# Kernel tuning notes

Hardware: AMD Instinct MI355X
Metric: run time of the kernel (lower is better)

## Reference

```python
import jax, jax.numpy as jnp
import numpy as np


def _seg_softmax(z, seg, num_seg):
    # PyG-style softmax over segments (numerically stable)
    m = jax.ops.segment_max(z, seg, num_segments=num_seg)
    e = jnp.exp(z - m[seg])
    s = jax.ops.segment_sum(e, seg, num_segments=num_seg)
    return e / s[seg]


def _structure(x, W, b, edge_index, batch):
    """Eager (numpy) watershed structure: peaks + level-synchronous BFS fill.
    Faithful to Clusterer.forward/fill: peaks are nodes whose elevation >= all
    in-neighbors; BFS expands along descending edges, a node joins the
    cluster(s) of whichever frontier origins reach it first (ties -> all),
    and is never re-assigned afterwards. Index structure is non-differentiable
    (matches torch autograd semantics)."""
    x = np.asarray(x); W = np.asarray(W); b = np.asarray(b)
    ei = np.asarray(edge_index); batch = np.asarray(batch)
    N = x.shape[0]; B = int(batch.max()) + 1
    # elevation = softmax(Linear(x), batch)
    z = (x @ W.T).ravel() + b[0]
    m = np.full(B, -np.inf, dtype=np.float64); np.maximum.at(m, batch, z)
    e = np.exp(z - m[batch]); s = np.zeros(B); np.add.at(s, batch, e)
    elev = e / s[batch]
    src, dst = ei[0], ei[1]
    # peaks: every incoming edge (src->dst) has elev[dst] >= elev[src]
    deg = np.bincount(dst, minlength=N)
    ge = np.bincount(dst[elev[dst] >= elev[src]], minlength=N)
    peaks = np.nonzero(ge == deg)[0]  # sorted, includes isolated nodes
    # descending edges only
    dmask = elev[dst] <= elev[src]
    ds, dd = src[dmask], dst[dmask]
    mems_list = [peaks]; ids_list = [peaks]
    visited = np.zeros(N, dtype=bool); visited[peaks] = True
    fn, fc = peaks, peaks  # frontier (node, cluster-id) pairs
    while fn.size:
        order = np.argsort(fn, kind='stable')
        fcs = fc[order]
        counts = np.bincount(fn, minlength=N)
        starts = np.concatenate([np.zeros(1, np.int64), np.cumsum(counts)])
        emask = counts[ds] > 0
        es, ed = ds[emask], dd[emask]
        rep = counts[es]
        tot = int(rep.sum())
        if tot == 0:
            break
        # attribute each descent edge to every cluster id of its origin
        base = np.repeat(starts[es], rep)
        grp = np.cumsum(rep) - rep
        within = np.arange(tot) - np.repeat(grp, rep)
        nc = fcs[base + within]
        nd = np.repeat(ed, rep)
        keep = ~visited[nd]  # nodes already in a cluster are never re-assigned
        nd, nc = nd[keep], nc[keep]
        if nd.size == 0:
            break
        pairs = np.unique(np.stack([nd, nc], axis=1), axis=0)
        nd, nc = pairs[:, 0], pairs[:, 1]
        visited[nd] = True
        mems_list.append(nd); ids_list.append(nc)
        fn, fc = nd, nc
    mems = np.concatenate(mems_list)
    ids = np.concatenate(ids_list)
    new_ids = np.searchsorted(peaks, ids)  # relabel peak node ids -> 0..P-1
    cluster_batch = batch[peaks]
    return mems, new_ids, peaks, cluster_batch, int(peaks.size), B


def setup_inputs() -> dict:
    rng = np.random.default_rng(0)
    N, C, B = 100000, 256, 8
    Ng = N // B
    Eu = 800000  # undirected edge draws, ~avg degree 16 after symmetrization
    g = rng.integers(0, B, Eu)
    s = g * Ng + rng.integers(0, Ng, Eu)
    d = g * Ng + rng.integers(0, Ng, Eu)
    keep = s != d
    s, d = s[keep], d[keep]
    src = np.concatenate([s, d]); dst = np.concatenate([d, s])
    key = src * N + dst
    _, idx = np.unique(key, return_index=True)  # coalesce (sorted, deduped)
    edge_index = np.stack([src[idx], dst[idx]]).astype(np.int64)
    batch = np.repeat(np.arange(B), Ng).astype(np.int64)
    x = rng.standard_normal((N, C)).astype(np.float32)
    W = (rng.standard_normal((1, C)) * 0.05).astype(np.float32)
    b = np.zeros((1,), np.float32)
    return {"x": jnp.asarray(x), "edge_index": jnp.asarray(edge_index),
            "batch": jnp.asarray(batch), "W": jnp.asarray(W), "b": jnp.asarray(b)}


def reference(x, edge_index, batch, W, b):
    mems, ids, peaks, cbatch, P, B = _structure(x, W, b, edge_index, batch)
    mems_j = jnp.asarray(mems); ids_j = jnp.asarray(ids); cb = jnp.asarray(cbatch)
    # differentiable pooling math (TopoPool.get_elevations + TopoPool.scale)
    z = (x @ W.T)[:, 0] + b[0]                       # [N]
    elev = _seg_softmax(z, batch, B)                  # per-graph softmax
    max_elev = jax.ops.segment_max(elev[mems_j], ids_j, num_segments=P)   # [P]
    max_x = jax.ops.segment_max(x[mems_j], ids_j, num_segments=P)        # [P,C]
    normed = _seg_softmax(max_elev, cb, B)            # softmax over clusters per graph
    pooled = max_x * normed[:, None]                  # [P,C]
    return pooled, cb, elev
```

## Files before the change

### kernel.cpp

```cpp
#include <hip/hip_runtime.h>
#include <hip/hip_bf16.h>
#include <stdint.h>


#define LINF 0x3FFFFFFF
#define MAXL 60
#define LSPLIT 10
#define NGMAX 12544
#define TAILCAP 8192

__device__ __forceinline__ unsigned encf(float f) {
  unsigned u = __float_as_uint(f);
  return (u & 0x80000000u) ? ~u : (u | 0x80000000u);
}
__device__ __forceinline__ float decf(unsigned u) {
  unsigned v = (u & 0x80000000u) ? (u & 0x7fffffffu) : ~u;
  return __uint_as_float(v);
}
__device__ __forceinline__ float bf2f(unsigned h) {
  return __uint_as_float(h << 16);
}
__device__ __forceinline__ unsigned f2bf(float f) {
  unsigned u = __float_as_uint(f);
  return (u + 0x7FFFu + ((u >> 16) & 1u)) >> 16;
}

__global__ void k_z(const float* __restrict__ x, const float* __restrict__ W,
                    const float* __restrict__ b, const int* __restrict__ batch,
                    float* __restrict__ z, unsigned* __restrict__ bmax_enc,
                    unsigned short* __restrict__ M, int N, int C) {
  __shared__ unsigned smax[8];
  if (threadIdx.x < 8) smax[threadIdx.x] = 0u;
  __syncthreads();
  int lane = threadIdx.x & 63;
  int wid = threadIdx.x >> 6;
  int chunk = (N + gridDim.x - 1) / gridDim.x;
  int v0 = blockIdx.x * chunk;
  int v1 = min(v0 + chunk, N);
  float b0 = b[0];
  for (int v = v0 + (wid << 2); v < v1; v += 16) {
    int nv = min(4, v1 - v);
    float acc[4] = {0.f, 0.f, 0.f, 0.f};
    for (int f = lane * 4; f < C; f += 256) {
      float4 xv[4];
      #pragma unroll
      for (int k = 0; k < 4; ++k) {
        int vv = v + (k < nv ? k : 0);
        xv[k] = *(const float4*)(x + (size_t)vv * C + f);
      }
      float4 wv = *(const float4*)(W + f);
      #pragma unroll
      for (int k = 0; k < 4; ++k) {
        acc[k] += xv[k].x * wv.x + xv[k].y * wv.y + xv[k].z * wv.z + xv[k].w * wv.w;
      }
      #pragma unroll
      for (int k = 0; k < 4; ++k) {
        if (k < nv) {
          uint2 pk;
          pk.x = f2bf(xv[k].x) | (f2bf(xv[k].y) << 16);
          pk.y = f2bf(xv[k].z) | (f2bf(xv[k].w) << 16);
          *(uint2*)(M + (size_t)(v + k) * C + f) = pk;
        }
      }
    }
    #pragma unroll
    for (int off = 32; off > 0; off >>= 1) {
      acc[0] += __shfl_xor(acc[0], off, 64);
      acc[1] += __shfl_xor(acc[1], off, 64);
      acc[2] += __shfl_xor(acc[2], off, 64);
      acc[3] += __shfl_xor(acc[3], off, 64);
    }
    if (lane < nv) {
      float zv = acc[lane] + b0;
      z[v + lane] = zv;
      atomicMax(&smax[batch[v + lane] & 7], encf(zv));
    }
  }
  __syncthreads();
  if (threadIdx.x < 8)
    if (smax[threadIdx.x]) atomicMax(&bmax_enc[threadIdx.x], smax[threadIdx.x]);
}

__global__ void k_e(const float* __restrict__ z, const int* __restrict__ batch,
                    const unsigned* __restrict__ bmax_enc, float* __restrict__ e,
                    float* __restrict__ bsum, int N) {
  __shared__ float ssum[1024];
  for (int i = threadIdx.x; i < 1024; i += blockDim.x) ssum[i] = 0.f;
  __syncthreads();
  int i = blockIdx.x * blockDim.x + threadIdx.x;
  if (i < N) {
    int bt = batch[i] & 1023;
    float ev = expf(z[i] - decf(bmax_enc[bt]));
    e[i] = ev;
    atomicAdd(&ssum[bt], ev);
  }
  __syncthreads();
  for (int t = threadIdx.x; t < 1024; t += blockDim.x)
    if (ssum[t] != 0.f) atomicAdd(&bsum[t], ssum[t]);
}

__global__ void k_edges(const int* __restrict__ ei, const float* __restrict__ z,
                        int* __restrict__ notpeak, int* __restrict__ desc_cnt,
                        const float* __restrict__ e, const float* __restrict__ bsum,
                        const int* __restrict__ batch, float* __restrict__ elev_out,
                        int E, int N) {
  int i = blockIdx.x * blockDim.x + threadIdx.x;
  if (i < N) elev_out[i] = e[i] / bsum[batch[i] & 1023];
  if (i >= E) return;
  int s = ei[i], d = ei[E + i];
  float zs = z[s], zd = z[d];
  if (zd < zs) notpeak[d] = 1;
  if (zd <= zs) atomicAdd(&desc_cnt[s], 1);
}

__global__ void k_chunksum2(const int* __restrict__ desc_cnt, const int* __restrict__ notpeak,
                            int n, int* __restrict__ csA, int* __restrict__ csB) {
  __shared__ int sA[512], sB[512];
  int t = threadIdx.x;
  int i = blockIdx.x * 512 + t;
  int a = 0, bb = 0;
  if (i < n) { a = desc_cnt[i]; bb = (notpeak[i] == 0) ? 1 : 0; }
  sA[t] = a; sB[t] = bb;
  __syncthreads();
  for (int off = 256; off > 0; off >>= 1) {
    if (t < off) { sA[t] += sA[t + off]; sB[t] += sB[t + off]; }
    __syncthreads();
  }
  if (t == 0) { csA[blockIdx.x] = sA[0]; csB[blockIdx.x] = sB[0]; }
}

__global__ void k_chunkscan2(int* __restrict__ csA, int* __restrict__ csB, int nchunks) {
  __shared__ int sA[1024], sB[1024];
  int t = threadIdx.x;
  int vA = (t < nchunks) ? csA[t] : 0;
  int vB = (t < nchunks) ? csB[t] : 0;
  sA[t] = vA; sB[t] = vB;
  __syncthreads();
  for (int off = 1; off < 1024; off <<= 1) {
    int aA = (t >= off) ? sA[t - off] : 0;
    int aB = (t >= off) ? sB[t - off] : 0;
    __syncthreads();
    sA[t] += aA; sB[t] += aB;
    __syncthreads();
  }
  if (t < nchunks) { csA[t] = sA[t] - vA; csB[t] = sB[t] - vB; }
}

__global__ void k_offsets(const int* __restrict__ vals, const int* __restrict__ chunkoff,
                          int2* __restrict__ ocp, int* __restrict__ cursor, int n) {
  __shared__ int s[512];
  int t = threadIdx.x;
  int i = blockIdx.x * 512 + t;
  int v = (i < n) ? vals[i] : 0;
  s[t] = v;
  __syncthreads();
  for (int off = 1; off < 512; off <<= 1) {
    int add = (t >= off) ? s[t - off] : 0;
    __syncthreads();
    s[t] += add;
    __syncthreads();
  }
  if (i < n) {
    int excl = s[t] - v + chunkoff[blockIdx.x];
    ocp[i] = make_int2(excl, excl);
    cursor[i] = excl;
  }
}

__global__ void k_peak_emit(const int* __restrict__ notpeak, const int* __restrict__ chunkoff,
                            const int* __restrict__ batch, const float* __restrict__ elev,
                            int* __restrict__ peaklist, int* __restrict__ cbatch,
                            float* __restrict__ out_cb, float* __restrict__ melev,
                            int n, int P) {
  __shared__ int s[512];
  int t = threadIdx.x;
  int i = blockIdx.x * 512 + t;
  int v = (i < n) ? (notpeak[i] == 0 ? 1 : 0) : 0;
  s[t] = v;
  __syncthreads();
  for (int off = 1; off < 512; off <<= 1) {
    int add = (t >= off) ? s[t - off] : 0;
    __syncthreads();
    s[t] += add;
    __syncthreads();
  }
  if (i < n && v) {
    int r = s[t] - 1 + chunkoff[blockIdx.x];
    if (r < P) {
      peaklist[r] = i;
      int bt = batch[i];
      cbatch[r] = bt;
      out_cb[r] = (float)bt;
      melev[r] = elev[i];
    }
  }
}

__global__ void k_fill(const int* __restrict__ ei, const float* __restrict__ z,
                       int* __restrict__ cursor, int* __restrict__ adj, int E) {
  int i = blockIdx.x * blockDim.x + threadIdx.x;
  if (i >= E) return;
  int s = ei[i], d = ei[E + i];
  if (z[d] <= z[s]) {
    int pos = atomicAdd(&cursor[s], 1);
    adj[pos] = d;
  }
}

__global__ void __launch_bounds__(1024, 1)
k_levels(const int* __restrict__ adj, const int2* __restrict__ ocp,
         const int* __restrict__ desc_cnt, const int* __restrict__ notpeak,
         int* __restrict__ level, int* __restrict__ lnodes,
         int* __restrict__ qend_g, int Ng, int N) {
  __shared__ int lvl[NGMAX];
  __shared__ unsigned short lq[NGMAX];
  __shared__ int soff[NGMAX + 1];
  __shared__ int s_qcnt[64];
  __shared__ int qend_s[64];
  const int b = blockIdx.x, base = b * Ng;
  const int tid = threadIdx.x, nth = blockDim.x;

  if (tid < 64) s_qcnt[tid] = 0;
  __syncthreads();
  for (int i = tid; i < Ng; i += nth) {
    soff[i] = ocp[base + i].x;
    bool pk = (notpeak[base + i] == 0);
    lvl[i] = pk ? 0 : LINF;
    if (pk) { int p = atomicAdd(&s_qcnt[0], 1); lq[p] = (unsigned short)i; }
  }
  if (tid == 0)
    soff[Ng] = (base + Ng < N) ? ocp[base + Ng].x : (ocp[N - 1].x + desc_cnt[N - 1]);
  __syncthreads();
  int qb = 0, qe = s_qcnt[0];
  int L = 0;
  while (L < MAXL && qe > qb) {
    if (tid == 0) qend_s[L] = qe;
    int units = (qe - qb) << 2;
    for (int t = tid; t < units; t += nth) {
      int qi = qb + (t >> 2), sub = t & 3;
      int lu = (int)lq[qi];
      int o = soff[lu], oe = soff[lu + 1];
      int j = o + sub;
      if (j < oe) {
        int w0 = adj[j];
        for (;;) {
          int jn = j + 4;
          int w1 = (jn < oe) ? adj[jn] : 0;
          int wl = w0 - base;
          if (lvl[wl] == LINF) {
            int old = atomicMin(&lvl[wl], L + 1);
            if (old == LINF) {
              int p = qe + atomicAdd(&s_qcnt[L + 1], 1);
              lq[p] = (unsigned short)wl;
            }
          }
          if (jn >= oe) break;
          w0 = w1; j = jn;
        }
      }
    }
    __syncthreads();
    int produced = s_qcnt[L + 1];
    qb = qe; qe += produced; ++L;
  }
  if (tid == 0) {
    for (int l = L; l < 63; ++l) qend_s[l] = qe;
    qend_s[63] = L;
  }
  __syncthreads();
  if (tid < 64) qend_g[b * 64 + tid] = qend_s[tid];
  for (int i = tid; i < Ng; i += nth) level[base + i] = lvl[i];
  for (int qi = tid; qi < qe; qi += nth) lnodes[base + qi] = (int)lq[qi];
}

__global__ void k_filter(const int* __restrict__ ei, const float* __restrict__ z,
                         const int* __restrict__ level, int2* __restrict__ ocp,
                         int* __restrict__ adj, int E) {
  int i = blockIdx.x * blockDim.x + threadIdx.x;
  if (i >= E) return;
  int s = ei[i], d = ei[E + i];
  if (z[d] <= z[s] && level[d] == level[s] + 1) {
    int pos = atomicAdd(&ocp[s].y, 1);
    adj[pos] = d;
  }
}

__global__ void __launch_bounds__(1024, 1)
k_dp_deep(const int* __restrict__ lnodes, const int* __restrict__ qend_g,
          const int2* __restrict__ ocp, const int* __restrict__ adj,
          unsigned short* __restrict__ M, int Ng, int C) {
  __shared__ unsigned short lqd[TAILCAP];
  __shared__ int2 soc[TAILCAP];
  __shared__ int qend_s[64];
  const int b = blockIdx.x, base = b * Ng;
  const int tid = threadIdx.x, nth = blockDim.x;
  if (tid < 64) qend_s[tid] = qend_g[b * 64 + tid];
  __syncthreads();
  const int Lmax = qend_s[63];
  if (Lmax - 1 < LSPLIT) return;
  const int ts = qend_s[LSPLIT - 1];
  const int qe = qend_s[62];
  const int tn = qe - ts;
  const bool useCache = (tn > 0) && (tn <= TAILCAP);
  if (useCache) {
    for (int i = tid; i < tn; i += nth) {
      int lid = lnodes[base + ts + i];
      lqd[i] = (unsigned short)lid;
      soc[i] = ocp[base + lid];
    }
  }
  __syncthreads();
  const int lane = tid & 31, hw = tid >> 5, nhw = nth >> 5;
  for (int L2 = Lmax - 1; L2 >= LSPLIT; --L2) {
    int sL = qend_s[L2 - 1], eL = qend_s[L2];
    for (int p = sL + hw; p < eL; p += nhw) {
      int u, o, e2;
      if (useCache) { u = base + (int)lqd[p - ts]; int2 v = soc[p - ts]; o = v.x; e2 = v.y; }
      else          { int lid = lnodes[base + p]; u = base + lid; int2 v = ocp[u]; o = v.x; e2 = v.y; }
      if (e2 == o) continue;
      uint4 sq = ((const uint4*)(M + (size_t)u * C))[lane];
      float4 a0, a1;
      a0.x = bf2f(sq.x & 0xffffu); a0.y = bf2f(sq.x >> 16);
      a0.z = bf2f(sq.y & 0xffffu); a0.w = bf2f(sq.y >> 16);
      a1.x = bf2f(sq.z & 0xffffu); a1.y = bf2f(sq.z >> 16);
      a1.z = bf2f(sq.w & 0xffffu); a1.w = bf2f(sq.w >> 16);
      for (int j = o; j < e2; ++j) {
        int wn = adj[j];
        uint4 q = ((const uint4*)(M + (size_t)wn * C))[lane];
        a0.x = fmaxf(a0.x, bf2f(q.x & 0xffffu));
        a0.y = fmaxf(a0.y, bf2f(q.x >> 16));
        a0.z = fmaxf(a0.z, bf2f(q.y & 0xffffu));
        a0.w = fmaxf(a0.w, bf2f(q.y >> 16));
        a1.x = fmaxf(a1.x, bf2f(q.z & 0xffffu));
        a1.y = fmaxf(a1.y, bf2f(q.z >> 16));
        a1.z = fmaxf(a1.z, bf2f(q.w & 0xffffu));
        a1.w = fmaxf(a1.w, bf2f(q.w >> 16));
      }
      uint4 pk4;
      pk4.x = f2bf(a0.x) | (f2bf(a0.y) << 16);
      pk4.y = f2bf(a0.z) | (f2bf(a0.w) << 16);
      pk4.z = f2bf(a1.x) | (f2bf(a1.y) << 16);
      pk4.w = f2bf(a1.z) | (f2bf(a1.w) << 16);
      ((uint4*)(M + (size_t)u * C))[lane] = pk4;
    }
    __syncthreads();
  }
}

__global__ void __launch_bounds__(256)
k_dp(const int* __restrict__ lnodes, const int* __restrict__ qend,
     const int* __restrict__ adj, const int2* __restrict__ ocp,
     unsigned short* __restrict__ M, int L, int C, int Ng) {
  const int b = blockIdx.y;
  int lane = threadIdx.x & 31;
  int ghw = (blockIdx.x * blockDim.x + threadIdx.x) >> 5;
  int nhw = (gridDim.x * blockDim.x) >> 5;
  int s = L ? qend[b * 64 + L - 1] : 0;
  int e = qend[b * 64 + L];
  for (int idx = s + ghw; idx < e; idx += nhw) {
    int u = b * Ng + lnodes[b * Ng + idx];
    int2 oc2 = ocp[u];
    int o = oc2.x, oc = oc2.y - oc2.x;
    if (oc == 0) continue;
    uint4 sq = ((const uint4*)(M + (size_t)u * C))[lane];
    float4 a0, a1;
    a0.x = bf2f(sq.x & 0xffffu); a0.y = bf2f(sq.x >> 16);
    a0.z = bf2f(sq.y & 0xffffu); a0.w = bf2f(sq.y >> 16);
    a1.x = bf2f(sq.z & 0xffffu); a1.y = bf2f(sq.z >> 16);
    a1.z = bf2f(sq.w & 0xffffu); a1.w = bf2f(sq.w >> 16);
    for (int j = 0; j < oc; j += 4) {
      int m = oc - j;
      int wn[4];
      #pragma unroll
      for (int k = 0; k < 4; k++) wn[k] = adj[o + j + (k < m ? k : 0)];
      #pragma unroll
      for (int k = 0; k < 4; k++) {
        uint4 q = ((const uint4*)(M + (size_t)wn[k] * C))[lane];
        a0.x = fmaxf(a0.x, bf2f(q.x & 0xffffu));
        a0.y = fmaxf(a0.y, bf2f(q.x >> 16));
        a0.z = fmaxf(a0.z, bf2f(q.y & 0xffffu));
        a0.w = fmaxf(a0.w, bf2f(q.y >> 16));
        a1.x = fmaxf(a1.x, bf2f(q.z & 0xffffu));
        a1.y = fmaxf(a1.y, bf2f(q.z >> 16));
        a1.z = fmaxf(a1.z, bf2f(q.w & 0xffffu));
        a1.w = fmaxf(a1.w, bf2f(q.w >> 16));
      }
    }
    uint4 p;
    p.x = f2bf(a0.x) | (f2bf(a0.y) << 16);
    p.y = f2bf(a0.z) | (f2bf(a0.w) << 16);
    p.z = f2bf(a1.x) | (f2bf(a1.y) << 16);
    p.w = f2bf(a1.z) | (f2bf(a1.w) << 16);
    ((uint4*)(M + (size_t)u * C))[lane] = p;
  }
}

__global__ void k_cnorm(const float* __restrict__ melev, const int* __restrict__ cbatch,
                        float* __restrict__ normed, int P) {
  __shared__ unsigned cm[1024];
  __shared__ float cs[1024];
  int t = threadIdx.x;
  for (int i = t; i < 1024; i += blockDim.x) { cm[i] = 0u; cs[i] = 0.f; }
  __syncthreads();
  for (int i = t; i < P; i += blockDim.x) atomicMax(&cm[cbatch[i] & 1023], encf(melev[i]));
  __syncthreads();
  for (int i = t; i < P; i += blockDim.x) {
    int bt = cbatch[i] & 1023;
    atomicAdd(&cs[bt], expf(melev[i] - decf(cm[bt])));
  }
  __syncthreads();
  for (int i = t; i < P; i += blockDim.x) {
    int bt = cbatch[i] & 1023;
    normed[i] = expf(melev[i] - decf(cm[bt])) / cs[bt];
  }
}

__global__ void __launch_bounds__(256)
k_dp0_pool(const int* __restrict__ peaklist, const float* __restrict__ normed,
           const int* __restrict__ adj, const int2* __restrict__ ocp,
           const unsigned short* __restrict__ M, float* __restrict__ out,
           int P, int C) {
  int lane = threadIdx.x & 31;
  int ghw = (blockIdx.x * blockDim.x + threadIdx.x) >> 5;
  int nhw = (gridDim.x * blockDim.x) >> 5;
  for (int r = ghw; r < P; r += nhw) {
    int u = peaklist[r];
    int2 oc2 = ocp[u];
    int o = oc2.x, oc = oc2.y - oc2.x;
    uint4 sq = ((const uint4*)(M + (size_t)u * C))[lane];
    float4 a0, a1;
    a0.x = bf2f(sq.x & 0xffffu); a0.y = bf2f(sq.x >> 16);
    a0.z = bf2f(sq.y & 0xffffu); a0.w = bf2f(sq.y >> 16);
    a1.x = bf2f(sq.z & 0xffffu); a1.y = bf2f(sq.z >> 16);
    a1.z = bf2f(sq.w & 0xffffu); a1.w = bf2f(sq.w >> 16);
    for (int j = 0; j < oc; j += 4) {
      int m = oc - j;
      int wn[4];
      #pragma unroll
      for (int k = 0; k < 4; k++) wn[k] = adj[o + j + (k < m ? k : 0)];
      #pragma unroll
      for (int k = 0; k < 4; k++) {
        uint4 q = ((const uint4*)(M + (size_t)wn[k] * C))[lane];
        a0.x = fmaxf(a0.x, bf2f(q.x & 0xffffu));
        a0.y = fmaxf(a0.y, bf2f(q.x >> 16));
        a0.z = fmaxf(a0.z, bf2f(q.y & 0xffffu));
        a0.w = fmaxf(a0.w, bf2f(q.y >> 16));
        a1.x = fmaxf(a1.x, bf2f(q.z & 0xffffu));
        a1.y = fmaxf(a1.y, bf2f(q.z >> 16));
        a1.z = fmaxf(a1.z, bf2f(q.w & 0xffffu));
        a1.w = fmaxf(a1.w, bf2f(q.w >> 16));
      }
    }
    float nr = normed[r];
    float* orow = out + (size_t)r * C + lane * 8;
    float4 o0 = make_float4(a0.x * nr, a0.y * nr, a0.z * nr, a0.w * nr);
    float4 o1 = make_float4(a1.x * nr, a1.y * nr, a1.z * nr, a1.w * nr);
    ((float4*)orow)[0] = o0;
    ((float4*)orow)[1] = o1;
  }
}

extern "C" void kernel_launch(void* const* d_in, const int* in_sizes, int n_in,
                              void* d_out, int out_size, void* d_ws, size_t ws_size,
                              hipStream_t stream) {
  const float* x = (const float*)d_in[0];
  const int* ei = (const int*)d_in[1];
  const int* batch = (const int*)d_in[2];
  const float* W = (const float*)d_in[3];
  const float* b = (const float*)d_in[4];

  const int N = in_sizes[2];
  const int C = in_sizes[0] / N;
  const int E = in_sizes[1] / 2;
  const int P = (out_size - N) / (C + 1);
  const int B = 8;
  const int Ng = N / B;

  float* out = (float*)d_out;
  float* out_pooled = out;
  float* out_cb = out + (size_t)P * C;
  float* out_elev = out_cb + P;

  char* w = (char*)d_ws;
  size_t off = 0;
  auto alloc = [&](size_t bytes) -> void* {
    off = (off + 255) & ~(size_t)255;
    void* p = (void*)(w + off);
    off += bytes;
    return p;
  };
  size_t zero_begin = 0;
  int* notpeak      = (int*)alloc((size_t)N * 4);
  int* desc_cnt     = (int*)alloc((size_t)N * 4);
  unsigned* bmax    = (unsigned*)alloc(1024 * 4);
  float* bsum       = (float*)alloc(1024 * 4);
  size_t zero_end = off;
  float* z          = (float*)alloc((size_t)N * 4);
  float* e          = (float*)alloc((size_t)N * 4);
  int2* ocp         = (int2*)alloc((size_t)N * 8);
  int* cursor       = (int*)alloc((size_t)N * 4);
  int* level        = (int*)alloc((size_t)N * 4);
  int* lnodes       = (int*)alloc((size_t)N * 4);
  int* qend         = (int*)alloc((size_t)B * 64 * 4);
  const int nchunks = (N + 511) / 512;
  int* csA          = (int*)alloc((size_t)nchunks * 4);
  int* csB          = (int*)alloc((size_t)nchunks * 4);
  int* cbatch       = (int*)alloc((size_t)P * 4);
  float* normed     = (float*)alloc((size_t)P * 4);
  float* melev      = (float*)alloc((size_t)P * 4);
  int* peaklist     = (int*)alloc((size_t)P * 4);
  int* adj          = (int*)alloc((size_t)E * 4);
  unsigned short* M = (unsigned short*)alloc((size_t)N * C * 2);

  hipMemsetAsync(w + zero_begin, 0, zero_end - zero_begin, stream);

  k_z<<<2048, 256, 0, stream>>>(x, W, b, batch, z, bmax, M, N, C);
  int nblkN = (N + 255) / 256;
  k_e<<<nblkN, 256, 0, stream>>>(z, batch, bmax, e, bsum, N);
  int nblkE = (E + 255) / 256;
  k_edges<<<nblkE, 256, 0, stream>>>(ei, z, notpeak, desc_cnt, e, bsum, batch,
                                     out_elev, E, N);
  k_chunksum2<<<nchunks, 512, 0, stream>>>(desc_cnt, notpeak, N, csA, csB);
  k_chunkscan2<<<1, 1024, 0, stream>>>(csA, csB, nchunks);
  k_offsets<<<nchunks, 512, 0, stream>>>(desc_cnt, csA, ocp, cursor, N);
  k_fill<<<nblkE, 256, 0, stream>>>(ei, z, cursor, adj, E);
  k_peak_emit<<<nchunks, 512, 0, stream>>>(notpeak, csB, batch, out_elev,
                                           peaklist, cbatch, out_cb, melev, N, P);
  k_cnorm<<<1, 1024, 0, stream>>>(melev, cbatch, normed, P);
  k_levels<<<B, 1024, 0, stream>>>(adj, ocp, desc_cnt, notpeak, level, lnodes,
                                   qend, Ng, N);
  k_filter<<<nblkE, 256, 0, stream>>>(ei, z, level, ocp, adj, E);
  k_dp_deep<<<B, 1024, 0, stream>>>(lnodes, qend, ocp, adj, M, Ng, C);
  dim3 gdp(256, B);
  for (int L = LSPLIT - 1; L >= 1; --L) {
    k_dp<<<gdp, 256, 0, stream>>>(lnodes, qend, adj, ocp, M, L, C, Ng);
  }
  k_dp0_pool<<<512, 256, 0, stream>>>(peaklist, normed, adj, ocp, M, out_pooled,
                                      P, C);
}
```

Measured before the change: 513.2 us.

## Store adjacency as 16-bit graph-local indices and prefetch edges in k_levels

Replaces the 32-bit global-index adjacency array with 16-bit indices local to each graph, rebuilding global indices from the graph base in the DP and pooling kernels. This halves adjacency memory traffic and footprint. It also adds a warm-up pass in k_levels that touches each graph's adjacency range so it is in cache before the serial BFS levels run. The change assumes every edge stays within one graph and that Ng fits in 16 bits. It adds a modulo in the fill kernels and a cbatch lookup in pooling.

```diff
diff --git a/kernel.cpp b/kernel.cpp
--- a/kernel.cpp
+++ b/kernel.cpp
@@ -197,18 +197,19 @@
 }
 
 __global__ void k_fill(const int* __restrict__ ei, const float* __restrict__ z,
-                       int* __restrict__ cursor, int* __restrict__ adj, int E) {
+                       int* __restrict__ cursor, unsigned short* __restrict__ adj16,
+                       int E, int Ng) {
   int i = blockIdx.x * blockDim.x + threadIdx.x;
   if (i >= E) return;
   int s = ei[i], d = ei[E + i];
   if (z[d] <= z[s]) {
     int pos = atomicAdd(&cursor[s], 1);
-    adj[pos] = d;
+    adj16[pos] = (unsigned short)(d % Ng);
   }
 }
 
 __global__ void __launch_bounds__(1024, 1)
-k_levels(const int* __restrict__ adj, const int2* __restrict__ ocp,
+k_levels(const unsigned short* __restrict__ adj16, const int2* __restrict__ ocp,
          const int* __restrict__ desc_cnt, const int* __restrict__ notpeak,
          int* __restrict__ level, int* __restrict__ lnodes,
          int* __restrict__ qend_g, int Ng, int N) {
@@ -230,6 +231,16 @@
   }
   if (tid == 0)
     soff[Ng] = (base + Ng < N) ? ocp[base + Ng].x : (ocp[N - 1].x + desc_cnt[N - 1]);
+  {
+    int e0 = ocp[base].x;
+    int e1 = (base + Ng < N) ? ocp[base + Ng].x : (ocp[N - 1].x + desc_cnt[N - 1]);
+    unsigned acc = 0;
+    const char* ap = (const char*)adj16;
+    for (long byteo = (long)e0 * 2 + (long)tid * 64; byteo < (long)e1 * 2;
+         byteo += (long)nth * 64)
+      acc += *(const unsigned*)(ap + (byteo & ~(long)3));
+    asm volatile("" :: "v"(acc));
+  }
   __syncthreads();
   int qb = 0, qe = s_qcnt[0];
   int L = 0;
@@ -242,11 +253,11 @@
       int o = soff[lu], oe = soff[lu + 1];
       int j = o + sub;
       if (j < oe) {
-        int w0 = adj[j];
+        int w0 = adj16[j];
         for (;;) {
           int jn = j + 4;
-          int w1 = (jn < oe) ? adj[jn] : 0;
-          int wl = w0 - base;
+          int w1 = (jn < oe) ? adj16[jn] : 0;
+          int wl = w0;
           if (lvl[wl] == LINF) {
             int old = atomicMin(&lvl[wl], L + 1);
             if (old == LINF) {
@@ -275,19 +286,19 @@
 
 __global__ void k_filter(const int* __restrict__ ei, const float* __restrict__ z,
                          const int* __restrict__ level, int2* __restrict__ ocp,
-                         int* __restrict__ adj, int E) {
+                         unsigned short* __restrict__ adj16, int E, int Ng) {
   int i = blockIdx.x * blockDim.x + threadIdx.x;
   if (i >= E) return;
   int s = ei[i], d = ei[E + i];
   if (z[d] <= z[s] && level[d] == level[s] + 1) {
     int pos = atomicAdd(&ocp[s].y, 1);
-    adj[pos] = d;
+    adj16[pos] = (unsigned short)(d % Ng);
   }
 }
 
 __global__ void __launch_bounds__(1024, 1)
 k_dp_deep(const int* __restrict__ lnodes, const int* __restrict__ qend_g,
-          const int2* __restrict__ ocp, const int* __restrict__ adj,
+          const int2* __restrict__ ocp, const unsigned short* __restrict__ adj16,
           unsigned short* __restrict__ M, int Ng, int C) {
   __shared__ unsigned short lqd[TAILCAP];
   __shared__ int2 soc[TAILCAP];
@@ -325,7 +336,7 @@
       a1.x = bf2f(sq.z & 0xffffu); a1.y = bf2f(sq.z >> 16);
       a1.z = bf2f(sq.w & 0xffffu); a1.w = bf2f(sq.w >> 16);
       for (int j = o; j < e2; ++j) {
-        int wn = adj[j];
+        int wn = base + (int)adj16[j];
         uint4 q = ((const uint4*)(M + (size_t)wn * C))[lane];
         a0.x = fmaxf(a0.x, bf2f(q.x & 0xffffu));
         a0.y = fmaxf(a0.y, bf2f(q.x >> 16));
@@ -349,16 +360,17 @@
 
 __global__ void __launch_bounds__(256)
 k_dp(const int* __restrict__ lnodes, const int* __restrict__ qend,
-     const int* __restrict__ adj, const int2* __restrict__ ocp,
+     const unsigned short* __restrict__ adj16, const int2* __restrict__ ocp,
      unsigned short* __restrict__ M, int L, int C, int Ng) {
   const int b = blockIdx.y;
+  const int bNg = b * Ng;
   int lane = threadIdx.x & 31;
   int ghw = (blockIdx.x * blockDim.x + threadIdx.x) >> 5;
   int nhw = (gridDim.x * blockDim.x) >> 5;
   int s = L ? qend[b * 64 + L - 1] : 0;
   int e = qend[b * 64 + L];
   for (int idx = s + ghw; idx < e; idx += nhw) {
-    int u = b * Ng + lnodes[b * Ng + idx];
+    int u = bNg + lnodes[bNg + idx];
     int2 oc2 = ocp[u];
     int o = oc2.x, oc = oc2.y - oc2.x;
     if (oc == 0) continue;
@@ -372,7 +384,8 @@
       int m = oc - j;
       int wn[4];
       #pragma unroll
-      for (int k = 0; k < 4; k++) wn[k] = adj[o + j + (k < m ? k : 0)];
+      for (int k = 0; k < 4; k++)
+        wn[k] = bNg + (int)adj16[o + j + (k < m ? k : 0)];
       #pragma unroll
       for (int k = 0; k < 4; k++) {
         uint4 q = ((const uint4*)(M + (size_t)wn[k] * C))[lane];
@@ -417,14 +430,15 @@
 
 __global__ void __launch_bounds__(256)
 k_dp0_pool(const int* __restrict__ peaklist, const float* __restrict__ normed,
-           const int* __restrict__ adj, const int2* __restrict__ ocp,
-           const unsigned short* __restrict__ M, float* __restrict__ out,
-           int P, int C) {
+           const unsigned short* __restrict__ adj16, const int2* __restrict__ ocp,
+           const int* __restrict__ cbatch, const unsigned short* __restrict__ M,
+           float* __restrict__ out, int P, int C, int Ng) {
   int lane = threadIdx.x & 31;
   int ghw = (blockIdx.x * blockDim.x + threadIdx.x) >> 5;
   int nhw = (gridDim.x * blockDim.x) >> 5;
   for (int r = ghw; r < P; r += nhw) {
     int u = peaklist[r];
+    int base = cbatch[r] * Ng;
     int2 oc2 = ocp[u];
     int o = oc2.x, oc = oc2.y - oc2.x;
     uint4 sq = ((const uint4*)(M + (size_t)u * C))[lane];
@@ -437,7 +451,8 @@
       int m = oc - j;
       int wn[4];
       #pragma unroll
-      for (int k = 0; k < 4; k++) wn[k] = adj[o + j + (k < m ? k : 0)];
+      for (int k = 0; k < 4; k++)
+        wn[k] = base + (int)adj16[o + j + (k < m ? k : 0)];
       #pragma unroll
       for (int k = 0; k < 4; k++) {
         uint4 q = ((const uint4*)(M + (size_t)wn[k] * C))[lane];
@@ -509,7 +524,7 @@
   float* normed     = (float*)alloc((size_t)P * 4);
   float* melev      = (float*)alloc((size_t)P * 4);
   int* peaklist     = (int*)alloc((size_t)P * 4);
-  int* adj          = (int*)alloc((size_t)E * 4);
+  unsigned short* adj16 = (unsigned short*)alloc((size_t)E * 2);
   unsigned short* M = (unsigned short*)alloc((size_t)N * C * 2);
 
   hipMemsetAsync(w + zero_begin, 0, zero_end - zero_begin, stream);
@@ -523,18 +538,18 @@
   k_chunksum2<<<nchunks, 512, 0, stream>>>(desc_cnt, notpeak, N, csA, csB);
   k_chunkscan2<<<1, 1024, 0, stream>>>(csA, csB, nchunks);
   k_offsets<<<nchunks, 512, 0, stream>>>(desc_cnt, csA, ocp, cursor, N);
-  k_fill<<<nblkE, 256, 0, stream>>>(ei, z, cursor, adj, E);
+  k_fill<<<nblkE, 256, 0, stream>>>(ei, z, cursor, adj16, E, Ng);
   k_peak_emit<<<nchunks, 512, 0, stream>>>(notpeak, csB, batch, out_elev,
                                            peaklist, cbatch, out_cb, melev, N, P);
   k_cnorm<<<1, 1024, 0, stream>>>(melev, cbatch, normed, P);
-  k_levels<<<B, 1024, 0, stream>>>(adj, ocp, desc_cnt, notpeak, level, lnodes,
+  k_levels<<<B, 1024, 0, stream>>>(adj16, ocp, desc_cnt, notpeak, level, lnodes,
                                    qend, Ng, N);
-  k_filter<<<nblkE, 256, 0, stream>>>(ei, z, level, ocp, adj, E);
-  k_dp_deep<<<B, 1024, 0, stream>>>(lnodes, qend, ocp, adj, M, Ng, C);
+  k_filter<<<nblkE, 256, 0, stream>>>(ei, z, level, ocp, adj16, E, Ng);
+  k_dp_deep<<<B, 1024, 0, stream>>>(lnodes, qend, ocp, adj16, M, Ng, C);
   dim3 gdp(256, B);
   for (int L = LSPLIT - 1; L >= 1; --L) {
-    k_dp<<<gdp, 256, 0, stream>>>(lnodes, qend, adj, ocp, M, L, C, Ng);
-  }
-  k_dp0_pool<<<512, 256, 0, stream>>>(peaklist, normed, adj, ocp, M, out_pooled,
-                                      P, C);
-}
+    k_dp<<<gdp, 256, 0, stream>>>(lnodes, qend, adj16, ocp, M, L, C, Ng);
+  }
+  k_dp0_pool<<<512, 256, 0, stream>>>(peaklist, normed, adj16, ocp, cbatch, M,
+                                      out_pooled, P, C, Ng);
+}
```

Result: faster. 498.2 us (-2.9%).
